# Kernel optimization log

Hardware: AMD Instinct MI355X
Metric: run time of the kernel (lower is better)

The kernel has to match this reference:

```python
import jax, jax.numpy as jnp
import numpy as np

E, D_IN, D_OUT, N = 8, 1024, 1024, 8192

def setup_inputs() -> dict:
    key = jax.random.key(0)
    ks = jax.random.split(key, 5)
    s_in = 1.0 / np.sqrt(D_IN)
    x = jax.random.normal(ks[0], (N, D_IN), dtype=jnp.float32)
    We = jax.random.uniform(ks[1], (E, D_IN, D_OUT), dtype=jnp.float32, minval=-s_in, maxval=s_in)
    be = jax.random.uniform(ks[2], (E, D_OUT), dtype=jnp.float32, minval=-s_in, maxval=s_in)
    Wg = jax.random.uniform(ks[3], (D_IN, E), dtype=jnp.float32, minval=-s_in, maxval=s_in)
    bg = jax.random.uniform(ks[4], (E,), dtype=jnp.float32, minval=-s_in, maxval=s_in)
    return {"x": x, "We": We, "be": be, "Wg": Wg, "bg": bg}

def reference(x, We, be, Wg, bg):
    # experts_outputs: [N, E, D_OUT] (stacked per-expert Linear outputs)
    expert_out = jnp.einsum('ni,eio->neo', x, We) + be[None, :, :]
    # gate: softmax over experts, [N, E]
    gate = jax.nn.softmax(x @ Wg + bg, axis=1)
    # weighted combine (bmm of [N,1,E] x [N,E,D_OUT]) -> [N, D_OUT]
    return jnp.einsum('ne,neo->no', gate, expert_out)
```

## Files before the change

### kernel.cpp

```cpp
#include <hip/hip_runtime.h>
#include <hip/hip_bf16.h>
#include <cstdint>

#define NTOK 8192
#define DIN  1024
#define DOUT 1024
#define NEXP 8

typedef __attribute__((ext_vector_type(8)))  __bf16 bf16x8;
typedef __attribute__((ext_vector_type(4)))  float  f32x4;

__device__ __forceinline__ unsigned short f2bf(float f) {
    unsigned int u = __builtin_bit_cast(unsigned int, f);
    u += 0x7FFFu + ((u >> 16) & 1u);
    return (unsigned short)(u >> 16);
}

__device__ __forceinline__ void cp16(const void* gsrc, void* ldst) {
    __builtin_amdgcn_global_load_lds(
        (const __attribute__((address_space(1))) void*)gsrc,
        (__attribute__((address_space(3))) void*)ldst,
        16, 0, 0);
}

#define BAR() asm volatile("s_barrier" ::: "memory")

__global__ __launch_bounds__(256) void prep_kernel(
    const float* __restrict__ x, const float* __restrict__ We,
    const float* __restrict__ Wg, const float* __restrict__ bg,
    unsigned short* __restrict__ xb, unsigned short* __restrict__ wt,
    float* __restrict__ g)
{
    __shared__ float smem[12416];

    int t = threadIdx.x;

    if (blockIdx.x < 2048) {
        unsigned short* tile = (unsigned short*)smem;
        int b = blockIdx.x;
        int e  = b >> 8;
        int kt = (b >> 4) & 15;
        int ot = b & 15;

        const float* src = We + ((size_t)e << 20) + (size_t)(kt * 64) * DOUT + ot * 64;
        unsigned short* dst = wt + ((size_t)e << 20) + (size_t)(ot * 64) * DIN + kt * 64;

        int kl = t >> 2;
        int og = (t & 3) * 16;
#pragma unroll
        for (int c = 0; c < 4; ++c) {
            int o = og + c * 4;
            float4 v = *(const float4*)&src[(size_t)kl * DOUT + o];
            ushort4 u;
            u.x = f2bf(v.x); u.y = f2bf(v.y); u.z = f2bf(v.z); u.w = f2bf(v.w);
            *(ushort4*)&tile[kl * 72 + o] = u;
        }
        __syncthreads();
        int ol = t >> 2;
        int kg = (t & 3) * 16;
        unsigned short tmp[16];
#pragma unroll
        for (int i = 0; i < 16; ++i) tmp[i] = tile[(kg + i) * 72 + ol];
        *(uint4*)&dst[(size_t)ol * DIN + kg]     = *(uint4*)&tmp[0];
        *(uint4*)&dst[(size_t)ol * DIN + kg + 8] = *(uint4*)&tmp[8];
    } else {
        float* WgL = smem;
        float* xL  = smem + 8192;
        int n0 = (blockIdx.x - 2048) * 32;

#pragma unroll
        for (int q = 0; q < 8; ++q) {
            int fidx = q * 256 + t;
            int k  = fidx >> 1;
            int eh = (fidx & 1) * 4;
            float4 v = *(const float4*)&Wg[(size_t)k * 8 + eh];
            WgL[(eh + 0) * 1024 + k] = v.x;
            WgL[(eh + 1) * 1024 + k] = v.y;
            WgL[(eh + 2) * 1024 + k] = v.z;
            WgL[(eh + 3) * 1024 + k] = v.w;
        }

        int tt = t & 31;
        int e  = t >> 5;
        float acc = 0.f;

        for (int c = 0; c < 8; ++c) {
            int kb = c * 128;
#pragma unroll
            for (int q = 0; q < 4; ++q) {
                int fidx = q * 256 + t;
                int row = fidx >> 5;
                int kk  = (fidx & 31) * 4;
                float4 v = *(const float4*)&x[(size_t)(n0 + row) * DIN + kb + kk];
                ushort4 u;
                u.x = f2bf(v.x); u.y = f2bf(v.y); u.z = f2bf(v.z); u.w = f2bf(v.w);
                *(ushort4*)&xb[(size_t)(n0 + row) * DIN + kb + kk] = u;
                *(float4*)&xL[row * 132 + kk] = v;
            }
            __syncthreads();
#pragma unroll
            for (int kk = 0; kk < 128; kk += 4) {
                float4 xv = *(const float4*)&xL[tt * 132 + kk];
                float4 wv = *(const float4*)&WgL[e * 1024 + kb + kk];
                acc += xv.x * wv.x + xv.y * wv.y + xv.z * wv.z + xv.w * wv.w;
            }
            __syncthreads();
        }

        float* lg = xL;
        lg[tt * 8 + e] = acc + bg[e];
        __syncthreads();
        if (t < 32) {
            float l[8];
#pragma unroll
            for (int i = 0; i < 8; ++i) l[i] = lg[t * 8 + i];
            float m = l[0];
#pragma unroll
            for (int i = 1; i < 8; ++i) m = fmaxf(m, l[i]);
            float s = 0.f;
#pragma unroll
            for (int i = 0; i < 8; ++i) { l[i] = __expf(l[i] - m); s += l[i]; }
            float inv = 1.0f / s;
            float4 p0 = make_float4(l[0]*inv, l[1]*inv, l[2]*inv, l[3]*inv);
            float4 p1 = make_float4(l[4]*inv, l[5]*inv, l[6]*inv, l[7]*inv);
            *(float4*)&g[(size_t)(n0 + tt) * 8]     = p0;
            *(float4*)&g[(size_t)(n0 + tt) * 8 + 4] = p1;
        }
    }
}

__global__ __launch_bounds__(512, 2) void moe_gemm_kernel(
    const unsigned short* __restrict__ xb,
    const unsigned short* __restrict__ wt,
    const float* __restrict__ g,
    const float* __restrict__ be,
    float* __restrict__ out)
{
    __shared__ unsigned short lA[2][256 * 64];
    __shared__ unsigned short lB[2][256 * 64];

    int bid = blockIdx.x;
    int xcd = bid & 7;
    int wl  = bid >> 3;
    int bn  = xcd * 4 + (wl & 3);
    int bm  = wl >> 2;

    int tid  = threadIdx.x;
    int lane = tid & 63;
    int wave = tid >> 6;
    int wm = wave >> 1;
    int wn = wave & 1;

    int rA   = lane & 15;
    int quad = lane >> 4;
    int swz  = rA & 7;
    int kp0  = (quad       ^ swz) << 3;
    int kp1  = ((quad + 4) ^ swz) << 3;

    int srow   = tid >> 3;
    int schunk = ((tid & 7) ^ (srow & 7)) << 3;
    int wOff   = wave * 512;

    const unsigned short* aBase = xb + (size_t)(bm * 256 + srow) * DIN + schunk;
    int eLo  = srow >> 5;
    int colB = srow & 31;
    const unsigned short* bBase = wt + (size_t)(bn * 32 + colB) * DIN + schunk;

#define STAGE_A(b, tt, H)                                                        \
    {   size_t ko = (size_t)(tt) * 64;                                           \
        cp16(aBase + (size_t)((H) * 128 +  0) * DIN + ko,                        \
             &lA[b][(H) * 8192 + 0 * 4096 + wOff]);                              \
        cp16(aBase + (size_t)((H) * 128 + 64) * DIN + ko,                        \
             &lA[b][(H) * 8192 + 1 * 4096 + wOff]); }
#define STAGE_B(b, tt, H)                                                        \
    {   size_t ko = (size_t)(tt) * 64;                                           \
        cp16(bBase + (((size_t)((H) * 4 + 0 + eLo)) << 20) + ko,                 \
             &lB[b][(H) * 8192 + 0 * 4096 + wOff]);                              \
        cp16(bBase + (((size_t)((H) * 4 + 2 + eLo)) << 20) + ko,                 \
             &lB[b][(H) * 8192 + 1 * 4096 + wOff]); }

    STAGE_A(0, 0, 0); STAGE_A(0, 0, 1);
    STAGE_B(0, 0, 0); STAGE_B(0, 0, 1);

    f32x4 acc[8][4] = {};

#pragma unroll 1
    for (int t = 0; t < 16; ++t) {
        int c = t & 1, n = c ^ 1;
        const unsigned short* A = lA[c];
        const unsigned short* B = lB[c];

        if (t < 15) { STAGE_A(n, t + 1, 0);
                      asm volatile("s_waitcnt vmcnt(2)" ::: "memory"); }
        else        { asm volatile("s_waitcnt vmcnt(0)" ::: "memory"); }
        BAR();

        bf16x8 af[4][2];
#pragma unroll
        for (int i = 0; i < 4; ++i) {
            af[i][0] = *(const bf16x8*)&A[(wm * 64 + i * 16 + rA) * 64 + kp0];
            af[i][1] = *(const bf16x8*)&A[(wm * 64 + i * 16 + rA) * 64 + kp1];
        }
        {
            bf16x8 b0h0 = *(const bf16x8*)&B[(0 * 32 + wn * 16 + rA) * 64 + kp0];
            bf16x8 b0h1 = *(const bf16x8*)&B[(0 * 32 + wn * 16 + rA) * 64 + kp1];
            bf16x8 b1h0 = *(const bf16x8*)&B[(1 * 32 + wn * 16 + rA) * 64 + kp0];
            bf16x8 b1h1 = *(const bf16x8*)&B[(1 * 32 + wn * 16 + rA) * 64 + kp1];
            __builtin_amdgcn_s_setprio(1);
#pragma unroll
            for (int i = 0; i < 4; ++i) {
                acc[0][i] = __builtin_amdgcn_mfma_f32_16x16x32_bf16(af[i][0], b0h0, acc[0][i], 0, 0, 0);
                acc[0][i] = __builtin_amdgcn_mfma_f32_16x16x32_bf16(af[i][1], b0h1, acc[0][i], 0, 0, 0);
                acc[1][i] = __builtin_amdgcn_mfma_f32_16x16x32_bf16(af[i][0], b1h0, acc[1][i], 0, 0, 0);
                acc[1][i] = __builtin_amdgcn_mfma_f32_16x16x32_bf16(af[i][1], b1h1, acc[1][i], 0, 0, 0);
            }
            __builtin_amdgcn_s_setprio(0);
        }
        BAR();

        if (t < 15) STAGE_A(n, t + 1, 1);
        {
            bf16x8 b0h0 = *(const bf16x8*)&B[(2 * 32 + wn * 16 + rA) * 64 + kp0];
            bf16x8 b0h1 = *(const bf16x8*)&B[(2 * 32 + wn * 16 + rA) * 64 + kp1];
            bf16x8 b1h0 = *(const bf16x8*)&B[(3 * 32 + wn * 16 + rA) * 64 + kp0];
            bf16x8 b1h1 = *(const bf16x8*)&B[(3 * 32 + wn * 16 + rA) * 64 + kp1];
            __builtin_amdgcn_s_setprio(1);
#pragma unroll
            for (int i = 0; i < 4; ++i) {
                acc[2][i] = __builtin_amdgcn_mfma_f32_16x16x32_bf16(af[i][0], b0h0, acc[2][i], 0, 0, 0);
                acc[2][i] = __builtin_amdgcn_mfma_f32_16x16x32_bf16(af[i][1], b0h1, acc[2][i], 0, 0, 0);
                acc[3][i] = __builtin_amdgcn_mfma_f32_16x16x32_bf16(af[i][0], b1h0, acc[3][i], 0, 0, 0);
                acc[3][i] = __builtin_amdgcn_mfma_f32_16x16x32_bf16(af[i][1], b1h1, acc[3][i], 0, 0, 0);
            }
            __builtin_amdgcn_s_setprio(0);
        }
        BAR();

        if (t < 15) STAGE_B(n, t + 1, 0);
        {
            bf16x8 b0h0 = *(const bf16x8*)&B[(4 * 32 + wn * 16 + rA) * 64 + kp0];
            bf16x8 b0h1 = *(const bf16x8*)&B[(4 * 32 + wn * 16 + rA) * 64 + kp1];
            bf16x8 b1h0 = *(const bf16x8*)&B[(5 * 32 + wn * 16 + rA) * 64 + kp0];
            bf16x8 b1h1 = *(const bf16x8*)&B[(5 * 32 + wn * 16 + rA) * 64 + kp1];
            __builtin_amdgcn_s_setprio(1);
#pragma unroll
            for (int i = 0; i < 4; ++i) {
                acc[4][i] = __builtin_amdgcn_mfma_f32_16x16x32_bf16(af[i][0], b0h0, acc[4][i], 0, 0, 0);
                acc[4][i] = __builtin_amdgcn_mfma_f32_16x16x32_bf16(af[i][1], b0h1, acc[4][i], 0, 0, 0);
                acc[5][i] = __builtin_amdgcn_mfma_f32_16x16x32_bf16(af[i][0], b1h0, acc[5][i], 0, 0, 0);
                acc[5][i] = __builtin_amdgcn_mfma_f32_16x16x32_bf16(af[i][1], b1h1, acc[5][i], 0, 0, 0);
            }
            __builtin_amdgcn_s_setprio(0);
        }
        BAR();

        if (t < 15) STAGE_B(n, t + 1, 1);
        {
            bf16x8 b0h0 = *(const bf16x8*)&B[(6 * 32 + wn * 16 + rA) * 64 + kp0];
            bf16x8 b0h1 = *(const bf16x8*)&B[(6 * 32 + wn * 16 + rA) * 64 + kp1];
            bf16x8 b1h0 = *(const bf16x8*)&B[(7 * 32 + wn * 16 + rA) * 64 + kp0];
            bf16x8 b1h1 = *(const bf16x8*)&B[(7 * 32 + wn * 16 + rA) * 64 + kp1];
            __builtin_amdgcn_s_setprio(1);
#pragma unroll
            for (int i = 0; i < 4; ++i) {
                acc[6][i] = __builtin_amdgcn_mfma_f32_16x16x32_bf16(af[i][0], b0h0, acc[6][i], 0, 0, 0);
                acc[6][i] = __builtin_amdgcn_mfma_f32_16x16x32_bf16(af[i][1], b0h1, acc[6][i], 0, 0, 0);
                acc[7][i] = __builtin_amdgcn_mfma_f32_16x16x32_bf16(af[i][0], b1h0, acc[7][i], 0, 0, 0);
                acc[7][i] = __builtin_amdgcn_mfma_f32_16x16x32_bf16(af[i][1], b1h1, acc[7][i], 0, 0, 0);
            }
            __builtin_amdgcn_s_setprio(0);
        }
        BAR();
    }

    int colg = bn * 32 + wn * 16 + rA;
    float bcol[8];
#pragma unroll
    for (int e = 0; e < 8; ++e) bcol[e] = be[(size_t)e * DOUT + colg];
#pragma unroll
    for (int i = 0; i < 4; ++i) {
        int rbase = bm * 256 + wm * 64 + i * 16 + quad * 4;
#pragma unroll
        for (int rr = 0; rr < 4; ++rr) {
            const float* gp = &g[(size_t)(rbase + rr) * 8];
            float4 g0 = *(const float4*)gp;
            float4 g1 = *(const float4*)(gp + 4);
            float s = g0.x * (acc[0][i][rr] + bcol[0])
                    + g0.y * (acc[1][i][rr] + bcol[1])
                    + g0.z * (acc[2][i][rr] + bcol[2])
                    + g0.w * (acc[3][i][rr] + bcol[3])
                    + g1.x * (acc[4][i][rr] + bcol[4])
                    + g1.y * (acc[5][i][rr] + bcol[5])
                    + g1.z * (acc[6][i][rr] + bcol[6])
                    + g1.w * (acc[7][i][rr] + bcol[7]);
            out[(size_t)(rbase + rr) * DOUT + colg] = s;
        }
    }
}

extern "C" void kernel_launch(void* const* d_in, const int* in_sizes, int n_in,
                              void* d_out, int out_size, void* d_ws, size_t ws_size,
                              hipStream_t stream)
{
    const float* x  = (const float*)d_in[0];
    const float* We = (const float*)d_in[1];
    const float* be = (const float*)d_in[2];
    const float* Wg = (const float*)d_in[3];
    const float* bg = (const float*)d_in[4];
    float* out = (float*)d_out;

    unsigned short* xb = (unsigned short*)d_ws;
    unsigned short* wt = xb + (size_t)NTOK * DIN;
    float* g = (float*)(wt + (size_t)NEXP * DOUT * DIN);

    prep_kernel<<<2048 + 256, 256, 0, stream>>>(x, We, Wg, bg, xb, wt, g);
    moe_gemm_kernel<<<(NTOK / 256) * (DOUT / 32), 512, 0, stream>>>(xb, wt, g, be, out);
}
```

Measured before the change: 261.8 us.

## Switch to 32x32x16 MFMA with expert-split waves and LDS combine reduction

Replaces the 16x16x32 MFMA tiling with 32x32x16 instructions. Each wave now owns 64 rows by 4 experts over the full 32-column tile instead of 64 rows by 16 columns across all 8 experts. The main loop is restructured into two MFMA phases per K-step, with fragment reads for the next half prefetched into registers and global staging batched per phase, which cuts barriers per iteration from four to two. Because experts are split across waves, the gated combine now needs an LDS reduction between wave pairs in the epilogue, adding a sync and LDS traffic.

```diff
diff --git a/kernel.cpp b/kernel.cpp
--- a/kernel.cpp
+++ b/kernel.cpp
@@ -9,6 +9,7 @@
 
 typedef __attribute__((ext_vector_type(8)))  __bf16 bf16x8;
 typedef __attribute__((ext_vector_type(4)))  float  f32x4;
+typedef __attribute__((ext_vector_type(16))) float  f32x16;
 
 __device__ __forceinline__ unsigned short f2bf(float f) {
     unsigned int u = __builtin_bit_cast(unsigned int, f);
@@ -148,14 +149,23 @@
     int tid  = threadIdx.x;
     int lane = tid & 63;
     int wave = tid >> 6;
-    int wm = wave >> 1;
-    int wn = wave & 1;
-
-    int rA   = lane & 15;
-    int quad = lane >> 4;
-    int swz  = rA & 7;
-    int kp0  = (quad       ^ swz) << 3;
-    int kp1  = ((quad + 4) ^ swz) << 3;
+    int wm   = wave >> 1;
+    int eg   = wave & 1;
+    int ebase = eg * 4;
+
+    int ln31 = lane & 31;
+    int kg   = lane >> 5;
+    int s    = ln31 & 7;
+
+    int kpo[4];
+#pragma unroll
+    for (int ks = 0; ks < 4; ++ks) kpo[ks] = (((ks * 2 + kg) ^ s) << 3);
+
+    int aRow[2], bRow[4];
+#pragma unroll
+    for (int mb = 0; mb < 2; ++mb) aRow[mb] = (wm * 64 + mb * 32 + ln31) * 64;
+#pragma unroll
+    for (int el = 0; el < 4; ++el) bRow[el] = ((ebase + el) * 32 + ln31) * 64;
 
     int srow   = tid >> 3;
     int schunk = ((tid & 7) ^ (srow & 7)) << 3;
@@ -179,10 +189,40 @@
         cp16(bBase + (((size_t)((H) * 4 + 2 + eLo)) << 20) + ko,                 \
              &lB[b][(H) * 8192 + 1 * 4096 + wOff]); }
 
+    bf16x8 af[2][2], bf[4][2];
+#define RD_FRAGS(Ab, Bb, kb)                                                     \
+    {                                                                            \
+        af[0][0] = *(const bf16x8*)&(Ab)[aRow[0] + kpo[(kb) + 0]];               \
+        af[1][0] = *(const bf16x8*)&(Ab)[aRow[1] + kpo[(kb) + 0]];               \
+        af[0][1] = *(const bf16x8*)&(Ab)[aRow[0] + kpo[(kb) + 1]];               \
+        af[1][1] = *(const bf16x8*)&(Ab)[aRow[1] + kpo[(kb) + 1]];               \
+        _Pragma("unroll")                                                        \
+        for (int el = 0; el < 4; ++el) {                                         \
+            bf[el][0] = *(const bf16x8*)&(Bb)[bRow[el] + kpo[(kb) + 0]];         \
+            bf[el][1] = *(const bf16x8*)&(Bb)[bRow[el] + kpo[(kb) + 1]];         \
+        }                                                                        \
+    }
+
+#define MFMA_PHASE()                                                             \
+    {   __builtin_amdgcn_s_setprio(1);                                           \
+        _Pragma("unroll")                                                        \
+        for (int q = 0; q < 2; ++q)                                              \
+            _Pragma("unroll")                                                    \
+            for (int el = 0; el < 4; ++el)                                       \
+                _Pragma("unroll")                                                \
+                for (int mb = 0; mb < 2; ++mb)                                   \
+                    acc[el][mb] = __builtin_amdgcn_mfma_f32_32x32x16_bf16(       \
+                        af[mb][q], bf[el][q], acc[el][mb], 0, 0, 0);             \
+        __builtin_amdgcn_s_setprio(0); }
+
     STAGE_A(0, 0, 0); STAGE_A(0, 0, 1);
     STAGE_B(0, 0, 0); STAGE_B(0, 0, 1);
 
-    f32x4 acc[8][4] = {};
+    f32x16 acc[4][2] = {};
+
+    asm volatile("s_waitcnt vmcnt(0)" ::: "memory");
+    BAR();
+    RD_FRAGS(lA[0], lB[0], 0);
 
 #pragma unroll 1
     for (int t = 0; t < 16; ++t) {
@@ -190,111 +230,59 @@
         const unsigned short* A = lA[c];
         const unsigned short* B = lB[c];
 
-        if (t < 15) { STAGE_A(n, t + 1, 0);
-                      asm volatile("s_waitcnt vmcnt(2)" ::: "memory"); }
-        else        { asm volatile("s_waitcnt vmcnt(0)" ::: "memory"); }
+        if (t < 15) { STAGE_A(n, t + 1, 0); STAGE_A(n, t + 1, 1); }
+        MFMA_PHASE();
+        RD_FRAGS(A, B, 2);
         BAR();
 
-        bf16x8 af[4][2];
-#pragma unroll
-        for (int i = 0; i < 4; ++i) {
-            af[i][0] = *(const bf16x8*)&A[(wm * 64 + i * 16 + rA) * 64 + kp0];
-            af[i][1] = *(const bf16x8*)&A[(wm * 64 + i * 16 + rA) * 64 + kp1];
-        }
-        {
-            bf16x8 b0h0 = *(const bf16x8*)&B[(0 * 32 + wn * 16 + rA) * 64 + kp0];
-            bf16x8 b0h1 = *(const bf16x8*)&B[(0 * 32 + wn * 16 + rA) * 64 + kp1];
-            bf16x8 b1h0 = *(const bf16x8*)&B[(1 * 32 + wn * 16 + rA) * 64 + kp0];
-            bf16x8 b1h1 = *(const bf16x8*)&B[(1 * 32 + wn * 16 + rA) * 64 + kp1];
-            __builtin_amdgcn_s_setprio(1);
-#pragma unroll
-            for (int i = 0; i < 4; ++i) {
-                acc[0][i] = __builtin_amdgcn_mfma_f32_16x16x32_bf16(af[i][0], b0h0, acc[0][i], 0, 0, 0);
-                acc[0][i] = __builtin_amdgcn_mfma_f32_16x16x32_bf16(af[i][1], b0h1, acc[0][i], 0, 0, 0);
-                acc[1][i] = __builtin_amdgcn_mfma_f32_16x16x32_bf16(af[i][0], b1h0, acc[1][i], 0, 0, 0);
-                acc[1][i] = __builtin_amdgcn_mfma_f32_16x16x32_bf16(af[i][1], b1h1, acc[1][i], 0, 0, 0);
+        if (t < 15) { STAGE_B(n, t + 1, 0); STAGE_B(n, t + 1, 1); }
+        MFMA_PHASE();
+        if (t < 15) asm volatile("s_waitcnt vmcnt(0)" ::: "memory");
+        BAR();
+        if (t < 15) RD_FRAGS(lA[n], lB[n], 0);
+    }
+
+    int colg = bn * 32 + ln31;
+    float bcol[4];
+#pragma unroll
+    for (int el = 0; el < 4; ++el)
+        bcol[el] = be[(size_t)(ebase + el) * DOUT + colg];
+
+    float part[2][16];
+#pragma unroll
+    for (int mb = 0; mb < 2; ++mb)
+#pragma unroll
+        for (int r = 0; r < 16; ++r) {
+            int rloc = mb * 32 + (r & 3) + 8 * (r >> 2) + 4 * kg;
+            int rowg = bm * 256 + wm * 64 + rloc;
+            float4 gv = *(const float4*)&g[(size_t)rowg * 8 + ebase];
+            part[mb][r] = gv.x * (acc[0][mb][r] + bcol[0])
+                        + gv.y * (acc[1][mb][r] + bcol[1])
+                        + gv.z * (acc[2][mb][r] + bcol[2])
+                        + gv.w * (acc[3][mb][r] + bcol[3]);
+        }
+
+    float* red = (float*)lA;
+    if (eg == 0) {
+#pragma unroll
+        for (int mb = 0; mb < 2; ++mb)
+#pragma unroll
+            for (int r = 0; r < 16; ++r) {
+                int rloc = mb * 32 + (r & 3) + 8 * (r >> 2) + 4 * kg;
+                red[wm * 2048 + rloc * 32 + ln31] = part[mb][r];
             }
-            __builtin_amdgcn_s_setprio(0);
-        }
-        BAR();
-
-        if (t < 15) STAGE_A(n, t + 1, 1);
-        {
-            bf16x8 b0h0 = *(const bf16x8*)&B[(2 * 32 + wn * 16 + rA) * 64 + kp0];
-            bf16x8 b0h1 = *(const bf16x8*)&B[(2 * 32 + wn * 16 + rA) * 64 + kp1];
-            bf16x8 b1h0 = *(const bf16x8*)&B[(3 * 32 + wn * 16 + rA) * 64 + kp0];
-            bf16x8 b1h1 = *(const bf16x8*)&B[(3 * 32 + wn * 16 + rA) * 64 + kp1];
-            __builtin_amdgcn_s_setprio(1);
-#pragma unroll
-            for (int i = 0; i < 4; ++i) {
-                acc[2][i] = __builtin_amdgcn_mfma_f32_16x16x32_bf16(af[i][0], b0h0, acc[2][i], 0, 0, 0);
-                acc[2][i] = __builtin_amdgcn_mfma_f32_16x16x32_bf16(af[i][1], b0h1, acc[2][i], 0, 0, 0);
-                acc[3][i] = __builtin_amdgcn_mfma_f32_16x16x32_bf16(af[i][0], b1h0, acc[3][i], 0, 0, 0);
-                acc[3][i] = __builtin_amdgcn_mfma_f32_16x16x32_bf16(af[i][1], b1h1, acc[3][i], 0, 0, 0);
+    }
+    __syncthreads();
+    if (eg == 1) {
+#pragma unroll
+        for (int mb = 0; mb < 2; ++mb)
+#pragma unroll
+            for (int r = 0; r < 16; ++r) {
+                int rloc = mb * 32 + (r & 3) + 8 * (r >> 2) + 4 * kg;
+                int rowg = bm * 256 + wm * 64 + rloc;
+                out[(size_t)rowg * DOUT + colg] =
+                    part[mb][r] + red[wm * 2048 + rloc * 32 + ln31];
             }
-            __builtin_amdgcn_s_setprio(0);
-        }
-        BAR();
-
-        if (t < 15) STAGE_B(n, t + 1, 0);
-        {
-            bf16x8 b0h0 = *(const bf16x8*)&B[(4 * 32 + wn * 16 + rA) * 64 + kp0];
-            bf16x8 b0h1 = *(const bf16x8*)&B[(4 * 32 + wn * 16 + rA) * 64 + kp1];
-            bf16x8 b1h0 = *(const bf16x8*)&B[(5 * 32 + wn * 16 + rA) * 64 + kp0];
-            bf16x8 b1h1 = *(const bf16x8*)&B[(5 * 32 + wn * 16 + rA) * 64 + kp1];
-            __builtin_amdgcn_s_setprio(1);
-#pragma unroll
-            for (int i = 0; i < 4; ++i) {
-                acc[4][i] = __builtin_amdgcn_mfma_f32_16x16x32_bf16(af[i][0], b0h0, acc[4][i], 0, 0, 0);
-                acc[4][i] = __builtin_amdgcn_mfma_f32_16x16x32_bf16(af[i][1], b0h1, acc[4][i], 0, 0, 0);
-                acc[5][i] = __builtin_amdgcn_mfma_f32_16x16x32_bf16(af[i][0], b1h0, acc[5][i], 0, 0, 0);
-                acc[5][i] = __builtin_amdgcn_mfma_f32_16x16x32_bf16(af[i][1], b1h1, acc[5][i], 0, 0, 0);
-            }
-            __builtin_amdgcn_s_setprio(0);
-        }
-        BAR();
-
-        if (t < 15) STAGE_B(n, t + 1, 1);
-        {
-            bf16x8 b0h0 = *(const bf16x8*)&B[(6 * 32 + wn * 16 + rA) * 64 + kp0];
-            bf16x8 b0h1 = *(const bf16x8*)&B[(6 * 32 + wn * 16 + rA) * 64 + kp1];
-            bf16x8 b1h0 = *(const bf16x8*)&B[(7 * 32 + wn * 16 + rA) * 64 + kp0];
-            bf16x8 b1h1 = *(const bf16x8*)&B[(7 * 32 + wn * 16 + rA) * 64 + kp1];
-            __builtin_amdgcn_s_setprio(1);
-#pragma unroll
-            for (int i = 0; i < 4; ++i) {
-                acc[6][i] = __builtin_amdgcn_mfma_f32_16x16x32_bf16(af[i][0], b0h0, acc[6][i], 0, 0, 0);
-                acc[6][i] = __builtin_amdgcn_mfma_f32_16x16x32_bf16(af[i][1], b0h1, acc[6][i], 0, 0, 0);
-                acc[7][i] = __builtin_amdgcn_mfma_f32_16x16x32_bf16(af[i][0], b1h0, acc[7][i], 0, 0, 0);
-                acc[7][i] = __builtin_amdgcn_mfma_f32_16x16x32_bf16(af[i][1], b1h1, acc[7][i], 0, 0, 0);
-            }
-            __builtin_amdgcn_s_setprio(0);
-        }
-        BAR();
-    }
-
-    int colg = bn * 32 + wn * 16 + rA;
-    float bcol[8];
-#pragma unroll
-    for (int e = 0; e < 8; ++e) bcol[e] = be[(size_t)e * DOUT + colg];
-#pragma unroll
-    for (int i = 0; i < 4; ++i) {
-        int rbase = bm * 256 + wm * 64 + i * 16 + quad * 4;
-#pragma unroll
-        for (int rr = 0; rr < 4; ++rr) {
-            const float* gp = &g[(size_t)(rbase + rr) * 8];
-            float4 g0 = *(const float4*)gp;
-            float4 g1 = *(const float4*)(gp + 4);
-            float s = g0.x * (acc[0][i][rr] + bcol[0])
-                    + g0.y * (acc[1][i][rr] + bcol[1])
-                    + g0.z * (acc[2][i][rr] + bcol[2])
-                    + g0.w * (acc[3][i][rr] + bcol[3])
-                    + g1.x * (acc[4][i][rr] + bcol[4])
-                    + g1.y * (acc[5][i][rr] + bcol[5])
-                    + g1.z * (acc[6][i][rr] + bcol[6])
-                    + g1.w * (acc[7][i][rr] + bcol[7]);
-            out[(size_t)(rbase + rr) * DOUT + colg] = s;
-        }
     }
 }
 
```

Measured after the change: 265.5 us. No clear change (+1.4%).
